# Optimization experiments

Measured on AMD Instinct MI355X. Metric: run time of the kernel, lower is better.

## Reference

```python
import jax, jax.numpy as jnp
import numpy as np

B, D, U = 256, 2048, 2048  # batch, input_dim, units
EPS = 1e-8


def setup_inputs() -> dict:
    key = jax.random.key(0)
    ks = jax.random.split(key, 20)
    sd = 1.0 / np.sqrt(D)
    su = 1.0 / np.sqrt(U)
    inp = {
        'x': jax.random.normal(ks[0], (B, D), jnp.float32),
        'h_prev': jax.random.normal(ks[1], (B, U), jnp.float32),
        'c_prev': jax.random.normal(ks[2], (B, U), jnp.float32),
        'n_prev': jax.random.uniform(ks[3], (B, U), jnp.float32),
        'm_prev': jax.random.normal(ks[4], (B, U), jnp.float32),
        # input-to-gate weights (Dense with bias), keras layout [in, out]
        'Wz': jax.random.normal(ks[5], (D, U), jnp.float32) * sd,
        'Wi': jax.random.normal(ks[6], (D, U), jnp.float32) * sd,
        'Wf': jax.random.normal(ks[7], (D, U), jnp.float32) * sd,
        'Wo': jax.random.normal(ks[8], (D, U), jnp.float32) * sd,
        'bz': jnp.zeros((U,), jnp.float32),
        'bi': jnp.zeros((U,), jnp.float32),
        'bf': jnp.zeros((U,), jnp.float32),
        'bo': jnp.zeros((U,), jnp.float32),
        # recurrent weights (Dense without bias)
        'Uz': jax.random.normal(ks[9], (U, U), jnp.float32) * su,
        'Ui': jax.random.normal(ks[10], (U, U), jnp.float32) * su,
        'Uf': jax.random.normal(ks[11], (U, U), jnp.float32) * su,
        'Uo': jax.random.normal(ks[12], (U, U), jnp.float32) * su,
    }
    return inp


def reference(x, h_prev, c_prev, n_prev, m_prev,
              Wz, Wi, Wf, Wo, bz, bi, bf, bo, Uz, Ui, Uf, Uo):
    # fuse the 8 small GEMMs into 2 wide GEMMs (same math, gates split after)
    W = jnp.concatenate([Wz, Wi, Wf, Wo], axis=1)      # [D, 4U]
    Uc = jnp.concatenate([Uz, Ui, Uf, Uo], axis=1)     # [U, 4U]
    b = jnp.concatenate([bz, bi, bf, bo], axis=0)      # [4U]
    pre = x @ W + h_prev @ Uc + b                      # [B, 4U]
    z_tilde, i_tilde, f_tilde, o_tilde = jnp.split(pre, 4, axis=1)

    # exponential-gate stabilization (forget_gate_type='exponential')
    m_t = jnp.maximum(i_tilde + m_prev, i_tilde)
    i_t = jnp.exp(i_tilde - m_t)
    f_t = jnp.exp(f_tilde + m_prev - m_t)

    o_t = jax.nn.sigmoid(o_tilde)
    z_t = jnp.tanh(z_tilde)

    c_t = f_t * c_prev + i_t * z_t
    n_t = f_t * n_prev + i_t
    h_t = o_t * (c_t / (n_t + EPS))
    return jnp.stack([h_t, c_t, n_t, m_t], axis=0)  # [4, B, U]
```

## Files before the change

### kernel.cpp

```cpp
#include <hip/hip_runtime.h>
#include <cstdint>
#include <cstddef>

#define B_   256
#define D_   2048
#define U_   2048
#define NTOT 8192
#define BN   32
#define BK   64
#define KC   2048
#define ITERS (KC / BK)

typedef _Float16 half8 __attribute__((ext_vector_type(8)));
typedef float floatx16 __attribute__((ext_vector_type(16)));

__global__ __launch_bounds__(256) void prep_kernel(
    const float* __restrict__ x, const float* __restrict__ h,
    _Float16* __restrict__ Ahi)
{
    int gid   = blockIdx.x * 256 + threadIdx.x;
    int chunk = gid >> 8;
    int row   = gid & 255;
    int col0  = chunk * 8;
    const float* src = (col0 < D_) ? (x + row * D_ + col0)
                                   : (h + row * U_ + (col0 - D_));
    float4 v0 = *(const float4*)(src);
    float4 v1 = *(const float4*)(src + 4);
    float v[8] = {v0.x, v0.y, v0.z, v0.w, v1.x, v1.y, v1.z, v1.w};
    half8 hi;
#pragma unroll
    for (int i = 0; i < 8; ++i) hi[i] = (_Float16)v[i];
    *(half8*)(Ahi + (chunk * 256 + row) * 8) = hi;
}

__global__ __launch_bounds__(256) void gemm_kernel(
    const _Float16* __restrict__ Ahi,
    const float* __restrict__ Wz, const float* __restrict__ Wi,
    const float* __restrict__ Wf, const float* __restrict__ Wo,
    const float* __restrict__ Uz, const float* __restrict__ Ui,
    const float* __restrict__ Uf, const float* __restrict__ Uo,
    float* __restrict__ P)
{
    __shared__ __align__(16) _Float16 sA[2][8 * 256 * 8];
    __shared__ __align__(16) float    sB[2][BK * BN];

    const int t    = threadIdx.x;
    const int w    = t >> 6;
    const int lane = t & 63;
    const int lg   = lane >> 5;
    const int lm   = lane & 31;

    const int nblk = blockIdx.x;
    const int ks   = blockIdx.y;
    const int n0   = nblk * BN;
    const int g    = n0 >> 11;
    const int c0   = n0 & (U_ - 1);

    const float* wsel[8] = {Wz, Wi, Wf, Wo, Uz, Ui, Uf, Uo};
    const float* Bm = wsel[ks * 4 + g];
    const int chunk0 = ks * 256;

    const int arow_t = t;
    const int bk_t   = t >> 3;
    const int bc_t   = (t & 7) * 4;

    floatx16 acc[2] = {};

#define STAGE(kk, buf)                                                        \
    {                                                                         \
        int gch = chunk0 + (kk) * 8;                                          \
        _Pragma("unroll")                                                     \
        for (int i = 0; i < 8; ++i) {                                         \
            int gidx = ((gch + i) * 256 + arow_t) * 8;                        \
            int lidx = (i * 256 + arow_t) * 8;                                \
            __builtin_amdgcn_global_load_lds(                                 \
                (const __attribute__((address_space(1))) void*)(Ahi + gidx),  \
                (__attribute__((address_space(3))) void*)(&sA[buf][lidx]),    \
                16, 0, 0);                                                    \
        }                                                                     \
        _Pragma("unroll")                                                     \
        for (int j = 0; j < 2; ++j) {                                         \
            int krow = j * 32 + bk_t;                                         \
            const float* src = Bm + (size_t)((kk) * BK + krow) * U_ + c0 + bc_t; \
            __builtin_amdgcn_global_load_lds(                                 \
                (const __attribute__((address_space(1))) void*)(src),         \
                (__attribute__((address_space(3))) void*)(&sB[buf][krow * BN + bc_t]), \
                16, 0, 0);                                                    \
        }                                                                     \
    }

    STAGE(0, 0);
    __syncthreads();

    for (int kk = 0; kk < ITERS; ++kk) {
        int cur = kk & 1;
        if (kk + 1 < ITERS) STAGE(kk + 1, cur ^ 1);

#pragma unroll
        for (int kin = 0; kin < 4; ++kin) {
            half8 a0, a1, bf;
            {
                int chunkIdx = kin * 2 + lg;
                int row0 = w * 64 + lm;
                a0 = *(const half8*)(&sA[cur][(chunkIdx * 256 + row0) * 8]);
                a1 = *(const half8*)(&sA[cur][(chunkIdx * 256 + row0 + 32) * 8]);
            }
#pragma unroll
            for (int j = 0; j < 8; ++j) {
                float v = sB[cur][(kin * 16 + lg * 8 + j) * BN + lm];
                bf[j] = (_Float16)v;
            }
            acc[0] = __builtin_amdgcn_mfma_f32_32x32x16_f16(a0, bf, acc[0], 0, 0, 0);
            acc[1] = __builtin_amdgcn_mfma_f32_32x32x16_f16(a1, bf, acc[1], 0, 0, 0);
        }
        __syncthreads();
    }
#undef STAGE

    float* Pks = P + (size_t)ks * ((size_t)B_ * NTOT);
#pragma unroll
    for (int mt = 0; mt < 2; ++mt)
#pragma unroll
        for (int r = 0; r < 16; ++r) {
            int m = w * 64 + mt * 32 + 4 * lg + (r & 3) + 8 * (r >> 2);
            Pks[(size_t)m * NTOT + n0 + lm] = acc[mt][r];
        }
}

__global__ __launch_bounds__(256) void gates_kernel(
    const float* __restrict__ P,
    const float* __restrict__ c_prev, const float* __restrict__ n_prev,
    const float* __restrict__ m_prev,
    const float* __restrict__ bz, const float* __restrict__ bi,
    const float* __restrict__ bf, const float* __restrict__ bo,
    float* __restrict__ out)
{
    const size_t PS = (size_t)B_ * NTOT;
    const int OS = B_ * U_;
    int gid = blockIdx.x * 256 + threadIdx.x;
    int m = gid >> 9;
    int u = (gid & 511) * 4;

    float pre[4][4];
#pragma unroll
    for (int gi = 0; gi < 4; ++gi) {
        const float* base = P + (size_t)m * NTOT + gi * U_ + u;
        float4 s0 = *(const float4*)(base);
        float4 s1 = *(const float4*)(base + PS);
        pre[gi][0] = s0.x + s1.x;
        pre[gi][1] = s0.y + s1.y;
        pre[gi][2] = s0.z + s1.z;
        pre[gi][3] = s0.w + s1.w;
    }
    float4 bzv = *(const float4*)(bz + u);
    float4 biv = *(const float4*)(bi + u);
    float4 bfv = *(const float4*)(bf + u);
    float4 bov = *(const float4*)(bo + u);
    float bza[4] = {bzv.x, bzv.y, bzv.z, bzv.w};
    float bia[4] = {biv.x, biv.y, biv.z, biv.w};
    float bfa[4] = {bfv.x, bfv.y, bfv.z, bfv.w};
    float boa[4] = {bov.x, bov.y, bov.z, bov.w};

    float4 cp4 = *(const float4*)(c_prev + m * U_ + u);
    float4 np4 = *(const float4*)(n_prev + m * U_ + u);
    float4 mp4 = *(const float4*)(m_prev + m * U_ + u);
    float cpa[4] = {cp4.x, cp4.y, cp4.z, cp4.w};
    float npa[4] = {np4.x, np4.y, np4.z, np4.w};
    float mpa[4] = {mp4.x, mp4.y, mp4.z, mp4.w};

    float hr[4], cr[4], nr[4], mr[4];
#pragma unroll
    for (int e = 0; e < 4; ++e) {
        float zt = pre[0][e] + bza[e];
        float it = pre[1][e] + bia[e];
        float ft = pre[2][e] + bfa[e];
        float ot = pre[3][e] + boa[e];
        float mp = mpa[e];
        float m_t = fmaxf(it + mp, it);
        float i_t = expf(it - m_t);
        float f_t = expf(ft + mp - m_t);
        float o_t = 1.0f / (1.0f + expf(-ot));
        float z_t = tanhf(zt);
        float c_t = f_t * cpa[e] + i_t * z_t;
        float n_t = f_t * npa[e] + i_t;
        float h_t = o_t * (c_t / (n_t + 1e-8f));
        hr[e] = h_t; cr[e] = c_t; nr[e] = n_t; mr[e] = m_t;
    }
    float4 hv = {hr[0], hr[1], hr[2], hr[3]};
    float4 cv = {cr[0], cr[1], cr[2], cr[3]};
    float4 nv = {nr[0], nr[1], nr[2], nr[3]};
    float4 mv = {mr[0], mr[1], mr[2], mr[3]};
    *(float4*)(out + 0 * OS + m * U_ + u) = hv;
    *(float4*)(out + 1 * OS + m * U_ + u) = cv;
    *(float4*)(out + 2 * OS + m * U_ + u) = nv;
    *(float4*)(out + 3 * OS + m * U_ + u) = mv;
}

extern "C" void kernel_launch(void* const* d_in, const int* in_sizes, int n_in,
                              void* d_out, int out_size, void* d_ws, size_t ws_size,
                              hipStream_t stream)
{
    const float* x  = (const float*)d_in[0];
    const float* h  = (const float*)d_in[1];
    const float* cp = (const float*)d_in[2];
    const float* np = (const float*)d_in[3];
    const float* mp = (const float*)d_in[4];
    const float* Wz = (const float*)d_in[5];
    const float* Wi = (const float*)d_in[6];
    const float* Wf = (const float*)d_in[7];
    const float* Wo = (const float*)d_in[8];
    const float* bz = (const float*)d_in[9];
    const float* bi = (const float*)d_in[10];
    const float* bf = (const float*)d_in[11];
    const float* bo = (const float*)d_in[12];
    const float* Uz = (const float*)d_in[13];
    const float* Ui = (const float*)d_in[14];
    const float* Uf = (const float*)d_in[15];
    const float* Uo = (const float*)d_in[16];

    float* P = (float*)d_ws;
    _Float16* Ahi = (_Float16*)((char*)d_ws + (size_t)2 * B_ * NTOT * sizeof(float));

    prep_kernel<<<512, 256, 0, stream>>>(x, h, Ahi);
    gemm_kernel<<<dim3(256, 2), 256, 0, stream>>>(Ahi,
        Wz, Wi, Wf, Wo, Uz, Ui, Uf, Uo, P);
    gates_kernel<<<512, 256, 0, stream>>>(P, cp, np, mp, bz, bi, bf, bo,
        (float*)d_out);
}
```

Measured before the change: 214.0 us.

## Load A fragments directly to registers and stage B as swizzled fp16 in LDS

Removes the large LDS staging buffer for the A operand. Each lane now loads its fp16 A fragments straight from global memory into registers, prefetching one step ahead. The B weights are loaded per thread through registers, converted to fp16 once, and written into a small XOR-swizzled LDS tile. This replaces the fp32 B tile that was converted on every read. The aim is to cut LDS footprint and raise occupancy (launch bounds now request 4 blocks), and to remove the repeated conversions and bank conflicts. In exchange, A is re-read from global or L2 by every wave, and the B loads become strided scalar loads.

```diff
diff --git a/kernel.cpp b/kernel.cpp
--- a/kernel.cpp
+++ b/kernel.cpp
@@ -33,7 +33,7 @@
     *(half8*)(Ahi + (chunk * 256 + row) * 8) = hi;
 }
 
-__global__ __launch_bounds__(256) void gemm_kernel(
+__global__ __launch_bounds__(256, 4) void gemm_kernel(
     const _Float16* __restrict__ Ahi,
     const float* __restrict__ Wz, const float* __restrict__ Wi,
     const float* __restrict__ Wf, const float* __restrict__ Wo,
@@ -41,8 +41,7 @@
     const float* __restrict__ Uf, const float* __restrict__ Uo,
     float* __restrict__ P)
 {
-    __shared__ __align__(16) _Float16 sA[2][8 * 256 * 8];
-    __shared__ __align__(16) float    sB[2][BK * BN];
+    __shared__ __align__(16) _Float16 sB[2][BK * BN];
 
     const int t    = threadIdx.x;
     const int w    = t >> 6;
@@ -60,62 +59,69 @@
     const float* Bm = wsel[ks * 4 + g];
     const int chunk0 = ks * 256;
 
-    const int arow_t = t;
-    const int bk_t   = t >> 3;
-    const int bc_t   = (t & 7) * 4;
+    const int scol = t & 31;
+    const int sk0  = (t >> 5) * 8;
+    const float* bsrc = Bm + (size_t)sk0 * U_ + c0 + scol;
+    const int swb = (scol * 128 + sk0 * 2) ^ ((scol & 7) << 4);
+
+    const _Float16* a0p = Ahi +
+        ((size_t)(chunk0 + lg) * 256 + (size_t)(w * 64 + lm)) * 8;
 
     floatx16 acc[2] = {};
 
-#define STAGE(kk, buf)                                                        \
-    {                                                                         \
-        int gch = chunk0 + (kk) * 8;                                          \
-        _Pragma("unroll")                                                     \
-        for (int i = 0; i < 8; ++i) {                                         \
-            int gidx = ((gch + i) * 256 + arow_t) * 8;                        \
-            int lidx = (i * 256 + arow_t) * 8;                                \
-            __builtin_amdgcn_global_load_lds(                                 \
-                (const __attribute__((address_space(1))) void*)(Ahi + gidx),  \
-                (__attribute__((address_space(3))) void*)(&sA[buf][lidx]),    \
-                16, 0, 0);                                                    \
-        }                                                                     \
-        _Pragma("unroll")                                                     \
-        for (int j = 0; j < 2; ++j) {                                         \
-            int krow = j * 32 + bk_t;                                         \
-            const float* src = Bm + (size_t)((kk) * BK + krow) * U_ + c0 + bc_t; \
-            __builtin_amdgcn_global_load_lds(                                 \
-                (const __attribute__((address_space(1))) void*)(src),         \
-                (__attribute__((address_space(3))) void*)(&sB[buf][krow * BN + bc_t]), \
-                16, 0, 0);                                                    \
-        }                                                                     \
-    }
-
-    STAGE(0, 0);
+    {
+        float v[8];
+#pragma unroll
+        for (int j = 0; j < 8; ++j) v[j] = bsrc[(size_t)j * U_];
+        half8 hv;
+#pragma unroll
+        for (int j = 0; j < 8; ++j) hv[j] = (_Float16)v[j];
+        *(half8*)((char*)(&sB[0][0]) + swb) = hv;
+    }
     __syncthreads();
 
+    half8 a0c = *(const half8*)(a0p);
+    half8 a1c = *(const half8*)(a0p + 256);
+
     for (int kk = 0; kk < ITERS; ++kk) {
-        int cur = kk & 1;
-        if (kk + 1 < ITERS) STAGE(kk + 1, cur ^ 1);
-
+        const int cur = kk & 1;
+
+        float bv[8];
+        if (kk + 1 < ITERS) {
+            const float* s = bsrc + (size_t)(kk + 1) * BK * U_;
+#pragma unroll
+            for (int j = 0; j < 8; ++j) bv[j] = s[(size_t)j * U_];
+        }
+
+        half8 bf[4];
 #pragma unroll
         for (int kin = 0; kin < 4; ++kin) {
-            half8 a0, a1, bf;
-            {
-                int chunkIdx = kin * 2 + lg;
-                int row0 = w * 64 + lm;
-                a0 = *(const half8*)(&sA[cur][(chunkIdx * 256 + row0) * 8]);
-                a1 = *(const half8*)(&sA[cur][(chunkIdx * 256 + row0 + 32) * 8]);
-            }
-#pragma unroll
-            for (int j = 0; j < 8; ++j) {
-                float v = sB[cur][(kin * 16 + lg * 8 + j) * BN + lm];
-                bf[j] = (_Float16)v;
-            }
-            acc[0] = __builtin_amdgcn_mfma_f32_32x32x16_f16(a0, bf, acc[0], 0, 0, 0);
-            acc[1] = __builtin_amdgcn_mfma_f32_32x32x16_f16(a1, bf, acc[1], 0, 0, 0);
+            int byte = (lm * 128 + (kin * 16 + lg * 8) * 2) ^ ((lm & 7) << 4);
+            bf[kin] = *(const half8*)((const char*)(&sB[cur][0]) + byte);
+        }
+
+        const _Float16* akk = a0p + (size_t)kk * 8 * 2048;
+        const int kknext = (kk + 1 < ITERS) ? (kk + 1) : 0;
+#pragma unroll
+        for (int kin = 0; kin < 4; ++kin) {
+            const _Float16* np = (kin < 3)
+                ? (akk + (size_t)(kin + 1) * 2 * 2048)
+                : (a0p + (size_t)kknext * 8 * 2048);
+            half8 a0n = *(const half8*)np;
+            half8 a1n = *(const half8*)(np + 256);
+            acc[0] = __builtin_amdgcn_mfma_f32_32x32x16_f16(a0c, bf[kin], acc[0], 0, 0, 0);
+            acc[1] = __builtin_amdgcn_mfma_f32_32x32x16_f16(a1c, bf[kin], acc[1], 0, 0, 0);
+            a0c = a0n; a1c = a1n;
+        }
+
+        if (kk + 1 < ITERS) {
+            half8 hv;
+#pragma unroll
+            for (int j = 0; j < 8; ++j) hv[j] = (_Float16)bv[j];
+            *(half8*)((char*)(&sB[cur ^ 1][0]) + swb) = hv;
         }
         __syncthreads();
     }
-#undef STAGE
 
     float* Pks = P + (size_t)ks * ((size_t)B_ * NTOT);
 #pragma unroll
```

Measured after the change: 261.1 us. 22.0% more time.
